# Performance work log

Hardware: AMD Instinct MI355X
Metric: run time of the kernel (lower is better)

Reference implementation:

```python
import jax, jax.numpy as jnp
import numpy as np

NUM_HEAD = 16
DIM = 1024
T, B = 2048, 4


def setup_inputs() -> dict:
    key = jax.random.key(0)
    ks = jax.random.split(key, 12)
    s = 1.0 / np.sqrt(DIM)
    return {
        "x1": jax.random.normal(ks[0], (T, B, DIM), jnp.float32),
        "x2": jax.random.normal(ks[1], (T, B, DIM), jnp.float32),
        "Wq": jax.random.normal(ks[2], (DIM, DIM), jnp.float32) * s,
        "bq": jax.random.normal(ks[3], (DIM,), jnp.float32) * 0.01,
        "Wk": jax.random.normal(ks[4], (DIM, DIM), jnp.float32) * s,
        "bk": jax.random.normal(ks[5], (DIM,), jnp.float32) * 0.01,
        "Wv": jax.random.normal(ks[6], (DIM, DIM), jnp.float32) * s,
        "bv": jax.random.normal(ks[7], (DIM,), jnp.float32) * 0.01,
        "Wu": jax.random.normal(ks[8], (DIM, DIM), jnp.float32) * s,
        "bu": jax.random.normal(ks[9], (DIM,), jnp.float32) * 0.01,
    }


def reference(x1, x2, Wq, bq, Wk, bk, Wv, bv, Wu, bu):
    T1, B1, C = x1.shape
    T2 = x2.shape[0]
    H = NUM_HEAD
    hd = C // H
    # (T,B,C) -> (B,T,C)
    x1b = jnp.transpose(x1, (1, 0, 2))
    x2b = jnp.transpose(x2, (1, 0, 2))
    # torch Linear: y = x @ W.T + b
    q = (x1b @ Wq.T + bq).reshape(B1, T1, H, hd).transpose(0, 2, 1, 3)  # (B,H,T1,hd)
    k = (x2b @ Wk.T + bk).reshape(B1, T2, H, hd).transpose(0, 2, 1, 3)
    v = (x2b @ Wv.T + bv).reshape(B1, T2, H, hd).transpose(0, 2, 1, 3)
    # NOTE: source scales by 1/sqrt(C) (full dim), not 1/sqrt(head_dim)
    attn = jnp.einsum("bhqd,bhkd->bhqk", q, k) / jnp.sqrt(jnp.asarray(C, q.dtype))
    attn = jax.nn.softmax(attn, axis=-1)
    # dropout = identity (eval mode, deterministic reference)
    out = jnp.einsum("bhqk,bhkd->bhqd", attn, v)  # (B,H,T1,hd)
    out = out.transpose(0, 2, 1, 3).reshape(B1, T1, C)  # merge heads
    out = out @ Wu.T + bu
    return out
```

## Files before the change

kernel.cpp:

```cpp
#include <hip/hip_runtime.h>

#define TSEQ 2048
#define BB 4
#define CDIM 1024
#define NH 16
#define HD 64
#define MR (TSEQ*BB)
#define C2SCALE 0.045084220f

typedef __attribute__((ext_vector_type(8))) short sh8;
typedef __attribute__((ext_vector_type(4))) short sh4;
typedef __attribute__((ext_vector_type(4))) float f4;
typedef __attribute__((ext_vector_type(4))) unsigned int u32x4;

__device__ __forceinline__ unsigned short f2bf(float x){
  unsigned u = __builtin_bit_cast(unsigned, x);
  u += 0x7fffu + ((u>>16)&1u);
  return (unsigned short)(u>>16);
}

__device__ __forceinline__ unsigned pk2(float a, float b){
  unsigned ua = __builtin_bit_cast(unsigned, a) + 0x8000u;
  unsigned ub = __builtin_bit_cast(unsigned, b) + 0x8000u;
  return __builtin_amdgcn_perm(ua, ub, 0x07060302u);
}

__device__ __forceinline__ void gll16(const unsigned short* g, unsigned short* l){
  __builtin_amdgcn_global_load_lds(
      (const __attribute__((address_space(1))) unsigned int*)g,
      (__attribute__((address_space(3))) unsigned int*)l, 16, 0, 0);
}

__global__ void conv_x(const float* __restrict__ a, const float* __restrict__ b,
                       unsigned short* __restrict__ ya, unsigned short* __restrict__ yb){
  const float* s = blockIdx.y ? b : a;
  unsigned short* d = blockIdx.y ? yb : ya;
  int i = (blockIdx.x*256 + threadIdx.x)*4;
  f4 v = *(const f4*)(s+i);
  sh4 o;
  o.x = (short)f2bf(v.x); o.y = (short)f2bf(v.y);
  o.z = (short)f2bf(v.z); o.w = (short)f2bf(v.w);
  *(sh4*)(d+i) = o;
}

__global__ void conv_w(const float* __restrict__ w0, const float* __restrict__ w1,
                       const float* __restrict__ w2, const float* __restrict__ w3,
                       unsigned short* __restrict__ y0, unsigned short* __restrict__ y1,
                       unsigned short* __restrict__ y2, unsigned short* __restrict__ y3){
  const float* s; unsigned short* d;
  switch(blockIdx.y){
    case 0: s=w0; d=y0; break;
    case 1: s=w1; d=y1; break;
    case 2: s=w2; d=y2; break;
    default: s=w3; d=y3; break;
  }
  int i = (blockIdx.x*256 + threadIdx.x)*4;
  f4 v = *(const f4*)(s+i);
  sh4 o;
  o.x = (short)f2bf(v.x); o.y = (short)f2bf(v.y);
  o.z = (short)f2bf(v.z); o.w = (short)f2bf(v.w);
  *(sh4*)(d+i) = o;
}

__global__ __launch_bounds__(256,2) void gemm_u(
    const unsigned short* __restrict__ A, const unsigned short* __restrict__ Bw,
    const float* __restrict__ bias, float* __restrict__ Cout){
  __shared__ unsigned short As[128*32];
  __shared__ unsigned short Bs[128*32];
  const int tid  = threadIdx.x;
  const int wave = tid>>6, lane = tid&63;
  const int g = lane>>4, c = lane&15;
  const int m0 = blockIdx.x*128, n0 = blockIdx.y*128;
  const int wr = wave>>1, wc = wave&1;
  f4 acc[4][4] = {};
  const int r0 = tid>>2, cc0 = tid&3;
  const unsigned short* Ag = A  + (size_t)(m0+r0)*CDIM + cc0*8;
  const unsigned short* Bg = Bw + (size_t)(n0+r0)*CDIM + cc0*8;

  for (int k0=0; k0<CDIM; k0+=32){
    __syncthreads();
    gll16(Ag + k0,                    As + tid*8);
    gll16(Ag + (size_t)64*CDIM + k0,  As + (256+tid)*8);
    gll16(Bg + k0,                    Bs + tid*8);
    gll16(Bg + (size_t)64*CDIM + k0,  Bs + (256+tid)*8);
    __syncthreads();
    sh8 af[4], bfr[4];
#pragma unroll
    for (int mt=0; mt<4; mt++) af[mt]  = *(const sh8*)(As + (wr*64+mt*16+c)*32 + g*8);
#pragma unroll
    for (int nt=0; nt<4; nt++) bfr[nt] = *(const sh8*)(Bs + (wc*64+nt*16+c)*32 + g*8);
#pragma unroll
    for (int mt=0; mt<4; mt++)
#pragma unroll
      for (int nt=0; nt<4; nt++)
        acc[mt][nt] = __builtin_amdgcn_mfma_f32_16x16x32_bf16(af[mt], bfr[nt], acc[mt][nt], 0,0,0);
  }

#pragma unroll
  for (int nt=0; nt<4; nt++){
    int nn = n0 + wc*64 + nt*16 + c;
    float bsv = bias[nn];
#pragma unroll
    for (int mt=0; mt<4; mt++){
      int mb = m0 + wr*64 + mt*16 + 4*g;
#pragma unroll
      for (int r=0; r<4; r++)
        Cout[(size_t)(mb+r)*CDIM + nn] = acc[mt][nt][r] + bsv;
    }
  }
}

__global__ __launch_bounds__(256,2) void gemm_qkv(
    const unsigned short* __restrict__ x1b, const unsigned short* __restrict__ x2b,
    const unsigned short* __restrict__ wq, const unsigned short* __restrict__ wk,
    const unsigned short* __restrict__ wv,
    const float* __restrict__ bq, const float* __restrict__ bk, const float* __restrict__ bv,
    unsigned short* __restrict__ Qo, unsigned short* __restrict__ Ko,
    unsigned short* __restrict__ Vo){
  __shared__ unsigned short As[128*32];
  __shared__ unsigned short Bs[128*32];
  const int z = blockIdx.z;
  const unsigned short* A  = (z==0) ? x1b : x2b;
  const unsigned short* Bw = (z==0) ? wq : (z==1) ? wk : wv;
  const float* bias        = (z==0) ? bq : (z==1) ? bk : bv;
  const int tid  = threadIdx.x;
  const int wave = tid>>6, lane = tid&63;
  const int g = lane>>4, c = lane&15;
  const int m0 = blockIdx.x*128, n0 = blockIdx.y*128;
  const int wr = wave>>1, wc = wave&1;
  f4 acc[4][4] = {};
  const int r0 = tid>>2, cc0 = tid&3;
  const unsigned short* Ag = A  + (size_t)(m0+r0)*CDIM + cc0*8;
  const unsigned short* Bg = Bw + (size_t)(n0+r0)*CDIM + cc0*8;

  for (int k0=0; k0<CDIM; k0+=32){
    __syncthreads();
    gll16(Ag + k0,                    As + tid*8);
    gll16(Ag + (size_t)64*CDIM + k0,  As + (256+tid)*8);
    gll16(Bg + k0,                    Bs + tid*8);
    gll16(Bg + (size_t)64*CDIM + k0,  Bs + (256+tid)*8);
    __syncthreads();
    sh8 af[4], bfr[4];
#pragma unroll
    for (int mt=0; mt<4; mt++) af[mt]  = *(const sh8*)(As + (wr*64+mt*16+c)*32 + g*8);
#pragma unroll
    for (int nt=0; nt<4; nt++) bfr[nt] = *(const sh8*)(Bs + (wc*64+nt*16+c)*32 + g*8);
#pragma unroll
    for (int mt=0; mt<4; mt++)
#pragma unroll
      for (int nt=0; nt<4; nt++)
        acc[mt][nt] = __builtin_amdgcn_mfma_f32_16x16x32_bf16(af[mt], bfr[nt], acc[mt][nt], 0,0,0);
  }

#pragma unroll
  for (int nt=0; nt<4; nt++){
    int nn = n0 + wc*64 + nt*16 + c;
    float bsv = bias[nn];
#pragma unroll
    for (int mt=0; mt<4; mt++){
      int mb = m0 + wr*64 + mt*16 + 4*g;
#pragma unroll
      for (int r=0; r<4; r++){
        float v = acc[mt][nt][r] + bsv;
        int mm = mb + r;
        if (z==0){
          Qo[(size_t)mm*CDIM + nn] = f2bf(v*C2SCALE);
        } else if (z==1){
          Ko[(size_t)mm*CDIM + nn] = f2bf(v);
        } else {
          int t = mm>>2, bb = mm&3, h = nn>>6, d = nn&63;
          Vo[(((size_t)bb*NH + h)*HD + d)*TSEQ + t] = f2bf(v);
        }
      }
    }
  }
}

__global__ __launch_bounds__(256,3) void attn_kernel(
    const unsigned short* __restrict__ Q, const unsigned short* __restrict__ Kb,
    const unsigned short* __restrict__ Vt, unsigned short* __restrict__ O){
  __shared__ unsigned short Ks[128*64];
  __shared__ unsigned short Vs[64*128];
  const int tid=threadIdx.x, wave=tid>>6, lane=tid&63;
  const int g=lane>>4, c=lane&15;
  const bool godd = (g&1);
  const int gx = blockIdx.x;
  const int bh = ((gx>>7)<<3) | (gx&7);
  const int qt = (gx>>3)&15;
  const int b = bh>>4, h = bh&15;
  const int qbase = qt*128 + wave*32;

  const unsigned short* kbase[4];
  const unsigned short* vbase[4];
#pragma unroll
  for (int i=0; i<4; i++){
    int cc = i*256+tid;
    int krow = cc>>3, kch = (cc&7) ^ (krow&7);
    kbase[i] = Kb + ((size_t)krow*BB + b)*CDIM + h*HD + kch*8;
    int vd = cc>>4, vch = (cc&15) ^ (vd&15);
    vbase[i] = Vt + ((size_t)(b*NH+h)*HD + vd)*TSEQ + vch*8;
  }

  sh8 qfr[2][2];
#pragma unroll
  for (int qf=0; qf<2; qf++)
#pragma unroll
    for (int kc=0; kc<2; kc++){
      int t = qbase + qf*16 + c;
      qfr[qf][kc] = *(const sh8*)(Q + ((size_t)t*BB + b)*CDIM + h*HD + kc*32 + g*8);
    }

  f4 oacc[4][2] = {};
  float lrun[2] = {0.f, 0.f};

  f4 kreg[4], vreg[4];
#pragma unroll
  for (int i=0; i<4; i++){
    kreg[i] = *(const f4*)(kbase[i]);
    vreg[i] = *(const f4*)(vbase[i]);
  }
#pragma unroll
  for (int i=0; i<4; i++){
    *(f4*)(Ks + (i*256+tid)*8) = kreg[i];
    *(f4*)(Vs + (i*256+tid)*8) = vreg[i];
  }
  __syncthreads();

  for (int iter=0; iter<TSEQ/128; iter++){
    if (iter < TSEQ/128-1){
      int k0n = (iter+1)*128;
#pragma unroll
      for (int i=0; i<4; i++){
        kreg[i] = *(const f4*)(kbase[i] + (size_t)k0n*BB*CDIM);
        vreg[i] = *(const f4*)(vbase[i] + k0n);
      }
    }

#pragma unroll
    for (int half=0; half<2; half++){
      f4 sacc[4][2] = {};
      __builtin_amdgcn_s_setprio(1);
#pragma unroll
      for (int kfl=0; kfl<4; kfl++){
        int kf = half*4 + kfl;
        sh8 af[2];
#pragma unroll
        for (int kc=0; kc<2; kc++){
          int ch = (kc*4+g) ^ (c&7);
          af[kc] = *(const sh8*)(Ks + (kf*16+c)*64 + ch*8);
        }
#pragma unroll
        for (int kc=0; kc<2; kc++)
#pragma unroll
          for (int qf=0; qf<2; qf++)
            sacc[kfl][qf] = __builtin_amdgcn_mfma_f32_16x16x32_bf16(af[kc], qfr[qf][kc], sacc[kfl][qf],0,0,0);
      }
      __builtin_amdgcn_s_setprio(0);

#pragma unroll
      for (int kc2l=0; kc2l<2; kc2l++){
        const int kc2 = half*2 + kc2l;
        sh8 pf[2];
#pragma unroll
        for (int qf=0; qf<2; qf++){
          f4 sa = sacc[2*kc2l][qf];
          f4 sb = sacc[2*kc2l+1][qf];
          float pa0 = __builtin_amdgcn_exp2f(sa[0]);
          float pa1 = __builtin_amdgcn_exp2f(sa[1]);
          float pa2 = __builtin_amdgcn_exp2f(sa[2]);
          float pa3 = __builtin_amdgcn_exp2f(sa[3]);
          float pb0 = __builtin_amdgcn_exp2f(sb[0]);
          float pb1 = __builtin_amdgcn_exp2f(sb[1]);
          float pb2 = __builtin_amdgcn_exp2f(sb[2]);
          float pb3 = __builtin_amdgcn_exp2f(sb[3]);
          lrun[qf] += ((pa0+pa1)+(pa2+pa3)) + ((pb0+pb1)+(pb2+pb3));
          unsigned A0 = pk2(pa1, pa0);
          unsigned A1 = pk2(pa3, pa2);
          unsigned B0 = pk2(pb1, pb0);
          unsigned B1 = pk2(pb3, pb2);
          asm("v_permlane32_swap_b32 %0, %1" : "+v"(A0), "+v"(B0));
          asm("v_permlane32_swap_b32 %0, %1" : "+v"(A1), "+v"(B1));
          unsigned xA0 = (unsigned)__builtin_amdgcn_ds_swizzle((int)A0, 0x401F);
          unsigned xA1 = (unsigned)__builtin_amdgcn_ds_swizzle((int)A1, 0x401F);
          unsigned xB0 = (unsigned)__builtin_amdgcn_ds_swizzle((int)B0, 0x401F);
          unsigned xB1 = (unsigned)__builtin_amdgcn_ds_swizzle((int)B1, 0x401F);
          u32x4 pw;
          pw.x = godd ? xB0 : A0;
          pw.y = godd ? xB1 : A1;
          pw.z = godd ? B0  : xA0;
          pw.w = godd ? B1  : xA1;
          pf[qf] = __builtin_bit_cast(sh8, pw);
        }
        __builtin_amdgcn_s_setprio(1);
#pragma unroll
        for (int df=0; df<4; df++){
          int ch = (kc2*4+g) ^ c;
          sh8 vf = *(const sh8*)(Vs + (df*16+c)*128 + ch*8);
#pragma unroll
          for (int qf=0; qf<2; qf++)
            oacc[df][qf] = __builtin_amdgcn_mfma_f32_16x16x32_bf16(vf, pf[qf], oacc[df][qf],0,0,0);
        }
        __builtin_amdgcn_s_setprio(0);
      }
    }

    __syncthreads();
    if (iter < TSEQ/128-1){
#pragma unroll
      for (int i=0; i<4; i++){
        *(f4*)(Ks + (i*256+tid)*8) = kreg[i];
        *(f4*)(Vs + (i*256+tid)*8) = vreg[i];
      }
      __syncthreads();
    }
  }

#pragma unroll
  for (int qf=0; qf<2; qf++){
    lrun[qf] += __shfl_xor(lrun[qf], 16, 64);
    lrun[qf] += __shfl_xor(lrun[qf], 32, 64);
    float inv = 1.0f/lrun[qf];
    int t = qbase + qf*16 + c;
#pragma unroll
    for (int df=0; df<4; df++){
      uint2 pr;
      pr.x = pk2(oacc[df][qf][1]*inv, oacc[df][qf][0]*inv);
      pr.y = pk2(oacc[df][qf][3]*inv, oacc[df][qf][2]*inv);
      *(uint2*)(O + ((size_t)b*TSEQ + t)*CDIM + h*HD + df*16 + 4*g) = pr;
    }
  }
}

extern "C" void kernel_launch(void* const* d_in, const int* in_sizes, int n_in,
                              void* d_out, int out_size, void* d_ws, size_t ws_size,
                              hipStream_t stream){
  (void)in_sizes; (void)n_in; (void)out_size; (void)ws_size;
  const float* x1 = (const float*)d_in[0];
  const float* x2 = (const float*)d_in[1];
  const float* Wq = (const float*)d_in[2];
  const float* bq = (const float*)d_in[3];
  const float* Wk = (const float*)d_in[4];
  const float* bk = (const float*)d_in[5];
  const float* Wv = (const float*)d_in[6];
  const float* bv = (const float*)d_in[7];
  const float* Wu = (const float*)d_in[8];
  const float* bu = (const float*)d_in[9];

  unsigned short* ws = (unsigned short*)d_ws;
  size_t o = 0;
  unsigned short* x1b = ws + o; o += (size_t)MR*CDIM;
  unsigned short* x2b = ws + o; o += (size_t)MR*CDIM;
  unsigned short* wqb = ws + o; o += (size_t)CDIM*CDIM;
  unsigned short* wkb = ws + o; o += (size_t)CDIM*CDIM;
  unsigned short* wvb = ws + o; o += (size_t)CDIM*CDIM;
  unsigned short* wub = ws + o; o += (size_t)CDIM*CDIM;
  unsigned short* Qb  = ws + o; o += (size_t)MR*CDIM;
  unsigned short* Kbf = ws + o; o += (size_t)MR*CDIM;
  unsigned short* Vtb = ws + o; o += (size_t)MR*CDIM;
  unsigned short* Ob  = x1b;

  conv_x<<<dim3((MR*CDIM)/1024, 2),   256, 0, stream>>>(x1, x2, x1b, x2b);
  conv_w<<<dim3((CDIM*CDIM)/1024, 4), 256, 0, stream>>>(Wq, Wk, Wv, Wu, wqb, wkb, wvb, wub);

  gemm_qkv<<<dim3(MR/128, CDIM/128, 3), 256, 0, stream>>>(
      x1b, x2b, wqb, wkb, wvb, bq, bk, bv, Qb, Kbf, Vtb);
  attn_kernel<<<dim3(1024), 256, 0, stream>>>(Qb, Kbf, Vtb, Ob);
  gemm_u<<<dim3(MR/128, CDIM/128), 256, 0, stream>>>(Ob, wub, bu, (float*)d_out);
}
```

Before: 330.8 us.

## Rewrite projection GEMMs with triple-buffered swizzled LDS pipeline and 256x128 tiles

```diff
diff --git a/kernel.cpp b/kernel.cpp
--- a/kernel.cpp
+++ b/kernel.cpp
@@ -62,39 +62,123 @@
   *(sh4*)(d+i) = o;
 }
 
-__global__ __launch_bounds__(256,2) void gemm_u(
+#define NKT 16
+#define BUFS 24576
+
+__device__ __forceinline__ void gemm_core(
+    const unsigned short* __restrict__ Aglob, const unsigned short* __restrict__ Bglob,
+    unsigned short* smem, int m0, int n0, int tid, f4 (&acc)[4][4])
+{
+  const int wave = tid>>6, lane = tid&63;
+  const int g = lane>>4, c = lane&15;
+  const int wr = wave>>1, wc = wave&1;
+
+  const unsigned short* aSrc[4]; int aOff[4];
+  const unsigned short* bSrc[2]; int bOff[2];
+#pragma unroll
+  for (int i=0;i<4;i++){
+    int slot = i*512+tid; int row = slot>>3, ch = slot&7;
+    aSrc[i] = Aglob + (size_t)(m0+row)*CDIM + (ch^(row&7))*8;
+    aOff[i] = slot*8;
+  }
+#pragma unroll
+  for (int i=0;i<2;i++){
+    int slot = i*512+tid; int row = slot>>3, ch = slot&7;
+    bSrc[i] = Bglob + (size_t)(n0+row)*CDIM + (ch^(row&7))*8;
+    bOff[i] = 16384 + slot*8;
+  }
+  const int arow = wr*64 + c;
+  const int brow = wc*64 + c;
+  const int ch0 = g ^ (c&7);
+  const int ch1 = (4+g) ^ (c&7);
+
+#pragma unroll
+  for (int i=0;i<4;i++) gll16(aSrc[i],     smem + aOff[i]);
+#pragma unroll
+  for (int i=0;i<2;i++) gll16(bSrc[i],     smem + bOff[i]);
+#pragma unroll
+  for (int i=0;i<4;i++) gll16(aSrc[i]+64,  smem + BUFS + aOff[i]);
+#pragma unroll
+  for (int i=0;i<2;i++) gll16(bSrc[i]+64,  smem + BUFS + bOff[i]);
+  asm volatile("s_waitcnt vmcnt(6)" ::: "memory");
+  __builtin_amdgcn_s_barrier();
+  __builtin_amdgcn_sched_barrier(0);
+
+  int q = 0;
+  for (int kt=0; kt<NKT; kt++){
+    unsigned short* bufc = smem + q*BUFS;
+    int r = q+2; if (r>=3) r-=3;
+    unsigned short* dst = smem + r*BUFS;
+    const int koff = (kt+2)*64;
+    sh8 af[4][2], bfr[2][2];
+#pragma unroll
+    for (int mt=0;mt<4;mt++){
+      af[mt][0] = *(const sh8*)(bufc + (arow+mt*16)*64 + ch0*8);
+      af[mt][1] = *(const sh8*)(bufc + (arow+mt*16)*64 + ch1*8);
+    }
+#pragma unroll
+    for (int nt=0;nt<2;nt++){
+      bfr[nt][0] = *(const sh8*)(bufc + 16384 + (brow+nt*16)*64 + ch0*8);
+      bfr[nt][1] = *(const sh8*)(bufc + 16384 + (brow+nt*16)*64 + ch1*8);
+    }
+    if (kt+2 < NKT){
+#pragma unroll
+      for (int i=0;i<4;i++) gll16(aSrc[i]+koff, dst + aOff[i]);
+    }
+    __builtin_amdgcn_s_barrier();
+    __builtin_amdgcn_sched_barrier(0);
+    __builtin_amdgcn_s_setprio(1);
+#pragma unroll
+    for (int mt=0;mt<4;mt++)
+#pragma unroll
+      for (int nt=0;nt<2;nt++){
+        acc[mt][nt] = __builtin_amdgcn_mfma_f32_16x16x32_bf16(af[mt][0], bfr[nt][0], acc[mt][nt],0,0,0);
+        acc[mt][nt] = __builtin_amdgcn_mfma_f32_16x16x32_bf16(af[mt][1], bfr[nt][1], acc[mt][nt],0,0,0);
+      }
+    __builtin_amdgcn_s_setprio(0);
+    __builtin_amdgcn_s_barrier();
+    __builtin_amdgcn_sched_barrier(0);
+#pragma unroll
+    for (int nt=0;nt<2;nt++){
+      bfr[nt][0] = *(const sh8*)(bufc + 16384 + (brow+(nt+2)*16)*64 + ch0*8);
+      bfr[nt][1] = *(const sh8*)(bufc + 16384 + (brow+(nt+2)*16)*64 + ch1*8);
+    }
+    if (kt+2 < NKT){
+#pragma unroll
+      for (int i=0;i<2;i++) gll16(bSrc[i]+koff, dst + bOff[i]);
+    }
+    __builtin_amdgcn_s_barrier();
+    __builtin_amdgcn_sched_barrier(0);
+    __builtin_amdgcn_s_setprio(1);
+#pragma unroll
+    for (int mt=0;mt<4;mt++)
+#pragma unroll
+      for (int nt=0;nt<2;nt++){
+        acc[mt][nt+2] = __builtin_amdgcn_mfma_f32_16x16x32_bf16(af[mt][0], bfr[nt][0], acc[mt][nt+2],0,0,0);
+        acc[mt][nt+2] = __builtin_amdgcn_mfma_f32_16x16x32_bf16(af[mt][1], bfr[nt][1], acc[mt][nt+2],0,0,0);
+      }
+    __builtin_amdgcn_s_setprio(0);
+    if (kt < NKT-1){
+      if (kt < NKT-2) asm volatile("s_waitcnt vmcnt(6)" ::: "memory");
+      else            asm volatile("s_waitcnt vmcnt(0)" ::: "memory");
+    }
+    __builtin_amdgcn_s_barrier();
+    __builtin_amdgcn_sched_barrier(0);
+    q = (q==2)?0:q+1;
+  }
+}
+
+__global__ __launch_bounds__(512,2) void gemm_u(
     const unsigned short* __restrict__ A, const unsigned short* __restrict__ Bw,
     const float* __restrict__ bias, float* __restrict__ Cout){
-  __shared__ unsigned short As[128*32];
-  __shared__ unsigned short Bs[128*32];
+  __shared__ unsigned short smem[3*BUFS];
   const int tid  = threadIdx.x;
   const int wave = tid>>6, lane = tid&63;
   const int g = lane>>4, c = lane&15;
-  const int m0 = blockIdx.x*128, n0 = blockIdx.y*128;
+  const int m0 = blockIdx.x*256, n0 = blockIdx.y*128;
   const int wr = wave>>1, wc = wave&1;
   f4 acc[4][4] = {};
-  const int r0 = tid>>2, cc0 = tid&3;
-  const unsigned short* Ag = A  + (size_t)(m0+r0)*CDIM + cc0*8;
-  const unsigned short* Bg = Bw + (size_t)(n0+r0)*CDIM + cc0*8;
-
-  for (int k0=0; k0<CDIM; k0+=32){
-    __syncthreads();
-    gll16(Ag + k0,                    As + tid*8);
-    gll16(Ag + (size_t)64*CDIM + k0,  As + (256+tid)*8);
-    gll16(Bg + k0,                    Bs + tid*8);
-    gll16(Bg + (size_t)64*CDIM + k0,  Bs + (256+tid)*8);
-    __syncthreads();
-    sh8 af[4], bfr[4];
-#pragma unroll
-    for (int mt=0; mt<4; mt++) af[mt]  = *(const sh8*)(As + (wr*64+mt*16+c)*32 + g*8);
-#pragma unroll
-    for (int nt=0; nt<4; nt++) bfr[nt] = *(const sh8*)(Bs + (wc*64+nt*16+c)*32 + g*8);
-#pragma unroll
-    for (int mt=0; mt<4; mt++)
-#pragma unroll
-      for (int nt=0; nt<4; nt++)
-        acc[mt][nt] = __builtin_amdgcn_mfma_f32_16x16x32_bf16(af[mt], bfr[nt], acc[mt][nt], 0,0,0);
-  }
+  gemm_core(A, Bw, smem, m0, n0, tid, acc);
 
 #pragma unroll
   for (int nt=0; nt<4; nt++){
@@ -110,15 +194,14 @@
   }
 }
 
-__global__ __launch_bounds__(256,2) void gemm_qkv(
+__global__ __launch_bounds__(512,2) void gemm_qkv(
     const unsigned short* __restrict__ x1b, const unsigned short* __restrict__ x2b,
     const unsigned short* __restrict__ wq, const unsigned short* __restrict__ wk,
     const unsigned short* __restrict__ wv,
     const float* __restrict__ bq, const float* __restrict__ bk, const float* __restrict__ bv,
     unsigned short* __restrict__ Qo, unsigned short* __restrict__ Ko,
     unsigned short* __restrict__ Vo){
-  __shared__ unsigned short As[128*32];
-  __shared__ unsigned short Bs[128*32];
+  __shared__ unsigned short smem[3*BUFS];
   const int z = blockIdx.z;
   const unsigned short* A  = (z==0) ? x1b : x2b;
   const unsigned short* Bw = (z==0) ? wq : (z==1) ? wk : wv;
@@ -126,31 +209,10 @@
   const int tid  = threadIdx.x;
   const int wave = tid>>6, lane = tid&63;
   const int g = lane>>4, c = lane&15;
-  const int m0 = blockIdx.x*128, n0 = blockIdx.y*128;
+  const int m0 = blockIdx.x*256, n0 = blockIdx.y*128;
   const int wr = wave>>1, wc = wave&1;
   f4 acc[4][4] = {};
-  const int r0 = tid>>2, cc0 = tid&3;
-  const unsigned short* Ag = A  + (size_t)(m0+r0)*CDIM + cc0*8;
-  const unsigned short* Bg = Bw + (size_t)(n0+r0)*CDIM + cc0*8;
-
-  for (int k0=0; k0<CDIM; k0+=32){
-    __syncthreads();
-    gll16(Ag + k0,                    As + tid*8);
-    gll16(Ag + (size_t)64*CDIM + k0,  As + (256+tid)*8);
-    gll16(Bg + k0,                    Bs + tid*8);
-    gll16(Bg + (size_t)64*CDIM + k0,  Bs + (256+tid)*8);
-    __syncthreads();
-    sh8 af[4], bfr[4];
-#pragma unroll
-    for (int mt=0; mt<4; mt++) af[mt]  = *(const sh8*)(As + (wr*64+mt*16+c)*32 + g*8);
-#pragma unroll
-    for (int nt=0; nt<4; nt++) bfr[nt] = *(const sh8*)(Bs + (wc*64+nt*16+c)*32 + g*8);
-#pragma unroll
-    for (int mt=0; mt<4; mt++)
-#pragma unroll
-      for (int nt=0; nt<4; nt++)
-        acc[mt][nt] = __builtin_amdgcn_mfma_f32_16x16x32_bf16(af[mt], bfr[nt], acc[mt][nt], 0,0,0);
-  }
+  gemm_core(A, Bw, smem, m0, n0, tid, acc);
 
 #pragma unroll
   for (int nt=0; nt<4; nt++){
@@ -362,8 +424,8 @@
   conv_x<<<dim3((MR*CDIM)/1024, 2),   256, 0, stream>>>(x1, x2, x1b, x2b);
   conv_w<<<dim3((CDIM*CDIM)/1024, 4), 256, 0, stream>>>(Wq, Wk, Wv, Wu, wqb, wkb, wvb, wub);
 
-  gemm_qkv<<<dim3(MR/128, CDIM/128, 3), 256, 0, stream>>>(
+  gemm_qkv<<<dim3(MR/256, CDIM/128, 3), 512, 0, stream>>>(
       x1b, x2b, wqb, wkb, wvb, bq, bk, bv, Qb, Kbf, Vtb);
   attn_kernel<<<dim3(1024), 256, 0, stream>>>(Qb, Kbf, Vtb, Ob);
-  gemm_u<<<dim3(MR/128, CDIM/128), 256, 0, stream>>>(Ob, wub, bu, (float*)d_out);
-}
+  gemm_u<<<dim3(MR/256, CDIM/128), 512, 0, stream>>>(Ob, wub, bu, (float*)d_out);
+}
```

New measurement: 330.6 us. Within noise of the previous version (-0.1%).
